# Kernel optimization log

Hardware: AMD Instinct MI355X
Metric: run time of the kernel (lower is better)

Reference implementation:

```python
import jax, jax.numpy as jnp
import numpy as np

D_MODEL = 1024
N_HEADS = 16


def setup_inputs() -> dict:
    key = jax.random.key(0)
    ks = jax.random.split(key, 5)
    B, T, C = 4, 2048, D_MODEL
    x = jax.random.normal(ks[0], (B, T, C), dtype=jnp.float32)
    W_attn = jax.random.normal(ks[1], (C, 3 * C), dtype=jnp.float32) * (1.0 / np.sqrt(C))
    b_attn = jnp.zeros((3 * C,), dtype=jnp.float32)
    W_proj = jax.random.normal(ks[2], (C, C), dtype=jnp.float32) * (1.0 / np.sqrt(C))
    b_proj = jnp.zeros((C,), dtype=jnp.float32)
    return {"x": x, "W_attn": W_attn, "b_attn": b_attn, "W_proj": W_proj, "b_proj": b_proj}


def reference(x, W_attn, b_attn, W_proj, b_proj):
    B, T, C = x.shape
    H = N_HEADS
    hd = C // H
    qkv = x @ W_attn + b_attn                      # [B,T,3C]
    q, k, v = jnp.split(qkv, 3, axis=2)
    # [B,T,C] -> [B,H,T,hd]
    q = q.reshape(B, T, H, hd).transpose(0, 2, 1, 3)
    k = k.reshape(B, T, H, hd).transpose(0, 2, 1, 3)
    v = v.reshape(B, T, H, hd).transpose(0, 2, 1, 3)
    scale = 1.0 / jnp.sqrt(jnp.float32(hd))
    attn = jnp.einsum('bhqd,bhkd->bhqk', q, k) * scale
    causal = jnp.tril(jnp.ones((T, T), dtype=bool))
    attn = jnp.where(causal[None, None], attn, -jnp.inf)
    w = jax.nn.softmax(attn, axis=-1)
    ctx = jnp.einsum('bhqk,bhkd->bhqd', w, v)      # [B,H,T,hd]
    ctx = ctx.transpose(0, 2, 1, 3).reshape(B, T, C)
    return ctx @ W_proj + b_proj
```

## Files before the change

kernel.cpp:

```cpp
#include <hip/hip_runtime.h>
#include <hip/hip_bf16.h>

typedef __bf16 bf16x8 __attribute__((ext_vector_type(8)));
typedef __bf16 bf16x4 __attribute__((ext_vector_type(4)));
typedef float f32x4 __attribute__((ext_vector_type(4)));

#define MFMA(A, B, C) __builtin_amdgcn_mfma_f32_16x16x32_bf16((A), (B), (C), 0, 0, 0)

#if __has_builtin(__builtin_amdgcn_exp2f)
#define EXP2(x) __builtin_amdgcn_exp2f(x)
#else
#define EXP2(x) exp2f(x)
#endif

#define T_SEQ 2048
#define BATCH 4
#define CDIM  1024
#define HEADS 16
#define HD    64
#define MROWS (BATCH * T_SEQ)
#define QK_SCALE 0.18033688011112042f
#define KTILES (CDIM / 64)

__device__ __forceinline__ void async_ld16(const __bf16* g, __bf16* l) {
    __builtin_amdgcn_global_load_lds(
        (const __attribute__((address_space(1))) void*)g,
        (__attribute__((address_space(3))) void*)l, 16, 0, 0);
}

__global__ __launch_bounds__(256) void prep(const float* __restrict__ x,
                                            __bf16* __restrict__ xbf,
                                            const float* __restrict__ Wa,
                                            __bf16* __restrict__ Wat,
                                            const float* __restrict__ Wp,
                                            __bf16* __restrict__ qkv)
{
    __shared__ float tile[32][33];
    const int bid = blockIdx.x;
    if (bid < 4096) {
        long i = ((long)bid * 256 + threadIdx.x) * 8;
        f32x4 f0 = ((const f32x4*)(x + i))[0];
        f32x4 f1 = ((const f32x4*)(x + i))[1];
        bf16x8 v;
#pragma unroll
        for (int j = 0; j < 4; j++) { v[j] = (__bf16)f0[j]; v[4 + j] = (__bf16)f1[j]; }
        *(bf16x8*)(xbf + i) = v;
    } else if (bid < 7168) {
        const int bb = bid - 4096;
        const int tx = threadIdx.x & 31, ty = threadIdx.x >> 5;
        const int c0 = (bb % 96) * 32, r0 = (bb / 96) * 32;
#pragma unroll
        for (int i = 0; i < 4; i++)
            tile[ty + i * 8][tx] = Wa[(long)(r0 + ty + i * 8) * (3 * CDIM) + c0 + tx];
        __syncthreads();
#pragma unroll
        for (int i = 0; i < 4; i++)
            Wat[(long)(c0 + ty + i * 8) * CDIM + r0 + tx] = (__bf16)tile[tx][ty + i * 8];
    } else {
        const int bb = bid - 7168;
        const int tx = threadIdx.x & 31, ty = threadIdx.x >> 5;
        const int c0 = (bb % 32) * 32, r0 = (bb / 32) * 32;
#pragma unroll
        for (int i = 0; i < 4; i++)
            tile[ty + i * 8][tx] = Wp[(long)(r0 + ty + i * 8) * CDIM + c0 + tx];
        __syncthreads();
#pragma unroll
        for (int i = 0; i < 4; i++)
            qkv[(long)(c0 + ty + i * 8) * (3 * CDIM) + 2 * CDIM + r0 + tx] =
                (__bf16)tile[tx][ty + i * 8];
    }
}


#define QS_ALO(p, kt)                                                            \
    do {                                                                         \
        async_ld16(Asrc + (long)(kt) * 64, &Ab[p][sdst]);                        \
        async_ld16(Asrc + (long)128 * CDIM + (kt) * 64, &Ab[p][8192 + sdst]);    \
    } while (0)
#define QS_AHI(p, kt)                                                            \
    do {                                                                         \
        async_ld16(Asrc + (long)64 * CDIM + (kt) * 64, &Ab[p][4096 + sdst]);     \
        async_ld16(Asrc + (long)192 * CDIM + (kt) * 64, &Ab[p][12288 + sdst]);   \
    } while (0)
#define QS_B(p, kt)                                                              \
    do {                                                                         \
        async_ld16(Bsrc + (long)(kt) * 64, &Bb[p][sdst]);                        \
        async_ld16(Bsrc + (long)64 * CDIM + (kt) * 64, &Bb[p][4096 + sdst]);     \
        async_ld16(Bsrc + (long)128 * CDIM + (kt) * 64, &Bb[p][8192 + sdst]);    \
    } while (0)

__global__ __launch_bounds__(512, 2) void gemm_qkv(const __bf16* __restrict__ A,
                                                   const __bf16* __restrict__ Bt,
                                                   const float* __restrict__ bias,
                                                   __bf16* __restrict__ C,
                                                   __bf16* __restrict__ vt)
{
    __shared__ __attribute__((aligned(16))) __bf16 Ab[2][256 * 64];
    __shared__ __attribute__((aligned(16))) __bf16 Bb[2][192 * 64];

    const int bid = (int)blockIdx.x;
    const int swz = (bid & 7) * 64 + (bid >> 3);
    const int n0 = (swz & 15) * 192;
    const int m0 = (swz >> 4) * 256;

    const int t = threadIdx.x;
    const int wave = t >> 6, lane = t & 63;
    const int quad = lane >> 4, l15 = lane & 15;
    const int wm = wave >> 2, wn = wave & 3;

    const int srow = t >> 3;
    const int scol = ((t & 7) * 8) ^ ((srow & 7) << 3);
    const int sdst = srow * 64 + (t & 7) * 8;
    const __bf16* Asrc = A + (long)(m0 + srow) * CDIM + scol;
    const __bf16* Bsrc = Bt + (long)(n0 + srow) * CDIM + scol;

    const int kx0 = (quad * 8) ^ ((l15 & 7) << 3);
    const int kx1 = (32 + quad * 8) ^ ((l15 & 7) << 3);
    const int aro = (wm * 128 + l15) * 64;
    const int bro = (wn * 48 + l15) * 64;

    f32x4 acc[8][3] = {};
    bf16x8 A0[4][2], A1[4][2], B0[2][2], B1[2];

    QS_ALO(0, 0); QS_AHI(0, 0); QS_B(0, 0);
    QS_ALO(1, 1); QS_AHI(1, 1); QS_B(1, 1);
    asm volatile("s_waitcnt vmcnt(7)" ::: "memory");
    __builtin_amdgcn_s_barrier();
#pragma unroll
    for (int mf = 0; mf < 4; mf++) {
        A0[mf][0] = *(const bf16x8*)&Ab[0][aro + mf * 1024 + kx0];
        A0[mf][1] = *(const bf16x8*)&Ab[0][aro + mf * 1024 + kx1];
    }
#pragma unroll
    for (int nf = 0; nf < 2; nf++) {
        B0[nf][0] = *(const bf16x8*)&Bb[0][bro + nf * 1024 + kx0];
        B0[nf][1] = *(const bf16x8*)&Bb[0][bro + nf * 1024 + kx1];
    }

#pragma unroll 2
    for (int kt = 0; kt < KTILES; ++kt) {
        const int cur = kt & 1, nxt = cur ^ 1;

#pragma unroll
        for (int mf = 0; mf < 4; mf++) {
            A1[mf][0] = *(const bf16x8*)&Ab[cur][aro + 4096 + mf * 1024 + kx0];
            A1[mf][1] = *(const bf16x8*)&Ab[cur][aro + 4096 + mf * 1024 + kx1];
        }
        B1[0] = *(const bf16x8*)&Bb[cur][bro + 2048 + kx0];
        B1[1] = *(const bf16x8*)&Bb[cur][bro + 2048 + kx1];
        asm volatile("s_waitcnt lgkmcnt(10)" ::: "memory");
        __builtin_amdgcn_sched_barrier(0);
        __builtin_amdgcn_s_setprio(1);
#pragma unroll
        for (int mf = 0; mf < 4; mf++)
#pragma unroll
            for (int nf = 0; nf < 2; nf++) {
                acc[mf][nf] = MFMA(A0[mf][0], B0[nf][0], acc[mf][nf]);
                acc[mf][nf] = MFMA(A0[mf][1], B0[nf][1], acc[mf][nf]);
            }
        __builtin_amdgcn_s_setprio(0);
        asm volatile("s_waitcnt lgkmcnt(0)" ::: "memory");
        __builtin_amdgcn_sched_barrier(0);
        __builtin_amdgcn_s_setprio(1);
#pragma unroll
        for (int mf = 0; mf < 4; mf++)
#pragma unroll
            for (int nf = 0; nf < 2; nf++) {
                acc[4 + mf][nf] = MFMA(A1[mf][0], B0[nf][0], acc[4 + mf][nf]);
                acc[4 + mf][nf] = MFMA(A1[mf][1], B0[nf][1], acc[4 + mf][nf]);
            }
        __builtin_amdgcn_s_setprio(0);
        asm volatile("s_waitcnt vmcnt(0)" ::: "memory");
        __builtin_amdgcn_s_barrier();

        __builtin_amdgcn_s_setprio(1);
#pragma unroll
        for (int mf = 0; mf < 4; mf++) {
            acc[mf][2] = MFMA(A0[mf][0], B1[0], acc[mf][2]);
            acc[mf][2] = MFMA(A0[mf][1], B1[1], acc[mf][2]);
        }
        __builtin_amdgcn_s_setprio(0);
        if (kt + 1 < KTILES) {
#pragma unroll
            for (int mf = 0; mf < 4; mf++) {
                A0[mf][0] = *(const bf16x8*)&Ab[nxt][aro + mf * 1024 + kx0];
                A0[mf][1] = *(const bf16x8*)&Ab[nxt][aro + mf * 1024 + kx1];
            }
#pragma unroll
            for (int nf = 0; nf < 2; nf++) {
                B0[nf][0] = *(const bf16x8*)&Bb[nxt][bro + nf * 1024 + kx0];
                B0[nf][1] = *(const bf16x8*)&Bb[nxt][bro + nf * 1024 + kx1];
            }
        }
        if (kt + 2 < KTILES) { QS_ALO(cur, kt + 2); QS_AHI(cur, kt + 2); QS_B(cur, kt + 2); }
        __builtin_amdgcn_s_setprio(1);
#pragma unroll
        for (int mf = 0; mf < 4; mf++) {
            acc[4 + mf][2] = MFMA(A1[mf][0], B1[0], acc[4 + mf][2]);
            acc[4 + mf][2] = MFMA(A1[mf][1], B1[1], acc[4 + mf][2]);
        }
        __builtin_amdgcn_s_setprio(0);
    }

    const int bB = m0 >> 11;
    const int tb = (m0 & (T_SEQ - 1)) + wm * 128;
#pragma unroll
    for (int mf = 0; mf < 8; mf++) {
#pragma unroll
        for (int nf = 0; nf < 3; nf++) {
            const int colb = n0 + wn * 48 + nf * 16;
            const int col = colb + l15;
            const float bv = bias[col];
            if (colb >= 2 * CDIM) {
                __bf16* vdst = vt + (long)(bB * CDIM + col - 2 * CDIM) * T_SEQ
                             + tb + (mf >> 2) * 64 + (mf & 3) * 16 + quad * 4;
                bf16x4 pv;
#pragma unroll
                for (int r = 0; r < 4; r++) pv[r] = (__bf16)(acc[mf][nf][r] + bv);
                *(bf16x4*)vdst = pv;
            } else {
                const float sc = (col < CDIM) ? QK_SCALE : 1.0f;
#pragma unroll
                for (int r = 0; r < 4; r++) {
                    const int row = m0 + wm * 128 + (mf >> 2) * 64 + (mf & 3) * 16 + quad * 4 + r;
                    C[(long)row * (3 * CDIM) + col] = (__bf16)((acc[mf][nf][r] + bv) * sc);
                }
            }
        }
    }
}

#define PS_A(p, kt)                                                              \
    do {                                                                         \
        async_ld16(Asrc + (long)(kt) * 64, &Ab[p][sdst]);                        \
        async_ld16(Asrc + (long)64 * (3 * CDIM) + (kt) * 64, &Ab[p][4096 + sdst]); \
    } while (0)
#define PS_B(p, kt)                                                              \
    do {                                                                         \
        async_ld16(Bsrc + (long)(kt) * 64, &Bb[p][sdst]);                        \
        async_ld16(Bsrc + (long)64 * (3 * CDIM) + (kt) * 64, &Bb[p][4096 + sdst]); \
        async_ld16(Bsrc + (long)128 * (3 * CDIM) + (kt) * 64, &Bb[p][8192 + sdst]); \
        async_ld16(Bsrc + (long)192 * (3 * CDIM) + (kt) * 64, &Bb[p][12288 + sdst]); \
    } while (0)

__global__ __launch_bounds__(512, 2) void gemm_proj(const __bf16* __restrict__ A,
                                                    const float* __restrict__ bias,
                                                    float* __restrict__ C)
{
    __shared__ __attribute__((aligned(16))) __bf16 Ab[2][128 * 64];
    __shared__ __attribute__((aligned(16))) __bf16 Bb[2][256 * 64];

    const int bid = (int)blockIdx.x;
    const int swz = (bid & 7) * 32 + (bid >> 3);
    const int n0 = (swz & 3) * 256;
    const int m0 = (swz >> 2) * 128;

    const int t = threadIdx.x;
    const int wave = t >> 6, lane = t & 63;
    const int quad = lane >> 4, l15 = lane & 15;
    const int wm = wave >> 2, wn = wave & 3;

    const int srow = t >> 3;
    const int scol = ((t & 7) * 8) ^ ((srow & 7) << 3);
    const int sdst = srow * 64 + (t & 7) * 8;
    const __bf16* Asrc = A + (long)(m0 + srow) * (3 * CDIM) + scol;
    const __bf16* Bsrc = A + (long)(n0 + srow) * (3 * CDIM) + 2 * CDIM + scol;

    const int kx0 = (quad * 8) ^ ((l15 & 7) << 3);
    const int kx1 = (32 + quad * 8) ^ ((l15 & 7) << 3);
    const int aro = (wm * 64 + l15) * 64;
    const int bro = (wn * 64 + l15) * 64;

    f32x4 acc[4][4] = {};
    bf16x8 A0[2][2], A1[2][2], B0[2][2], B1[2][2];

    PS_A(0, 0); PS_B(0, 0);
    PS_A(1, 1); PS_B(1, 1);
    asm volatile("s_waitcnt vmcnt(6)" ::: "memory");
    __builtin_amdgcn_s_barrier();
#pragma unroll
    for (int mf = 0; mf < 2; mf++) {
        A0[mf][0] = *(const bf16x8*)&Ab[0][aro + mf * 1024 + kx0];
        A0[mf][1] = *(const bf16x8*)&Ab[0][aro + mf * 1024 + kx1];
    }
#pragma unroll
    for (int nf = 0; nf < 2; nf++) {
        B0[nf][0] = *(const bf16x8*)&Bb[0][bro + nf * 1024 + kx0];
        B0[nf][1] = *(const bf16x8*)&Bb[0][bro + nf * 1024 + kx1];
    }

#pragma unroll 2
    for (int kt = 0; kt < KTILES; ++kt) {
        const int cur = kt & 1, nxt = cur ^ 1;

#pragma unroll
        for (int mf = 0; mf < 2; mf++) {
            A1[mf][0] = *(const bf16x8*)&Ab[cur][aro + 2048 + mf * 1024 + kx0];
            A1[mf][1] = *(const bf16x8*)&Ab[cur][aro + 2048 + mf * 1024 + kx1];
        }
#pragma unroll
        for (int nf = 0; nf < 2; nf++) {
            B1[nf][0] = *(const bf16x8*)&Bb[cur][bro + 2048 + nf * 1024 + kx0];
            B1[nf][1] = *(const bf16x8*)&Bb[cur][bro + 2048 + nf * 1024 + kx1];
        }
        asm volatile("s_waitcnt lgkmcnt(8)" ::: "memory");
        __builtin_amdgcn_sched_barrier(0);
        __builtin_amdgcn_s_setprio(1);
#pragma unroll
        for (int mf = 0; mf < 2; mf++)
#pragma unroll
            for (int nf = 0; nf < 2; nf++) {
                acc[mf][nf] = MFMA(A0[mf][0], B0[nf][0], acc[mf][nf]);
                acc[mf][nf] = MFMA(A0[mf][1], B0[nf][1], acc[mf][nf]);
            }
        __builtin_amdgcn_s_setprio(0);
        asm volatile("s_waitcnt lgkmcnt(0)" ::: "memory");
        __builtin_amdgcn_sched_barrier(0);
        __builtin_amdgcn_s_setprio(1);
#pragma unroll
        for (int mf = 0; mf < 2; mf++)
#pragma unroll
            for (int nf = 0; nf < 2; nf++) {
                acc[2 + mf][nf] = MFMA(A1[mf][0], B0[nf][0], acc[2 + mf][nf]);
                acc[2 + mf][nf] = MFMA(A1[mf][1], B0[nf][1], acc[2 + mf][nf]);
            }
        __builtin_amdgcn_s_setprio(0);
        asm volatile("s_waitcnt vmcnt(0)" ::: "memory");
        __builtin_amdgcn_s_barrier();

        __builtin_amdgcn_s_setprio(1);
#pragma unroll
        for (int mf = 0; mf < 2; mf++)
#pragma unroll
            for (int nf = 0; nf < 2; nf++) {
                acc[mf][2 + nf] = MFMA(A0[mf][0], B1[nf][0], acc[mf][2 + nf]);
                acc[mf][2 + nf] = MFMA(A0[mf][1], B1[nf][1], acc[mf][2 + nf]);
            }
        __builtin_amdgcn_s_setprio(0);
        if (kt + 1 < KTILES) {
#pragma unroll
            for (int mf = 0; mf < 2; mf++) {
                A0[mf][0] = *(const bf16x8*)&Ab[nxt][aro + mf * 1024 + kx0];
                A0[mf][1] = *(const bf16x8*)&Ab[nxt][aro + mf * 1024 + kx1];
            }
#pragma unroll
            for (int nf = 0; nf < 2; nf++) {
                B0[nf][0] = *(const bf16x8*)&Bb[nxt][bro + nf * 1024 + kx0];
                B0[nf][1] = *(const bf16x8*)&Bb[nxt][bro + nf * 1024 + kx1];
            }
        }
        if (kt + 2 < KTILES) { PS_A(cur, kt + 2); PS_B(cur, kt + 2); }
        __builtin_amdgcn_s_setprio(1);
#pragma unroll
        for (int mf = 0; mf < 2; mf++)
#pragma unroll
            for (int nf = 0; nf < 2; nf++) {
                acc[2 + mf][2 + nf] = MFMA(A1[mf][0], B1[nf][0], acc[2 + mf][2 + nf]);
                acc[2 + mf][2 + nf] = MFMA(A1[mf][1], B1[nf][1], acc[2 + mf][2 + nf]);
            }
        __builtin_amdgcn_s_setprio(0);
    }

#pragma unroll
    for (int mf = 0; mf < 4; mf++) {
#pragma unroll
        for (int nf = 0; nf < 4; nf++) {
            const int col = n0 + wn * 64 + (nf >> 1) * 32 + (nf & 1) * 16 + l15;
            const float bv = bias[col];
#pragma unroll
            for (int r = 0; r < 4; r++) {
                const int row = m0 + wm * 64 + (mf >> 1) * 32 + (mf & 1) * 16 + quad * 4 + r;
                C[(long)row * CDIM + col] = acc[mf][nf][r] + bv;
            }
        }
    }
}

#define ATT_STAGE(p, kt_)                                                        \
    do {                                                                         \
        const __bf16* kp_ = kbase + (long)(kt_) * 64 * (3 * CDIM);               \
        async_ld16(kp_,      &Ks[p][0][t * 8]);                                  \
        async_ld16(kp_ + 32, &Ks[p][1][t * 8]);                                  \
        const __bf16* vp_ = vbase + (kt_) * 64;                                  \
        async_ld16(vp_,      &Vts[p][0][t * 8]);                                 \
        async_ld16(vp_ + 32, &Vts[p][1][t * 8]);                                 \
    } while (0)

__global__ __launch_bounds__(256, 3) void attn_kernel(__bf16* qkv,
                                                      const __bf16* __restrict__ vt)
{
    __shared__ __attribute__((aligned(16))) __bf16 Ks[2][2][64 * 32];
    __shared__ __attribute__((aligned(16))) __bf16 Vts[2][2][64 * 32];
    __shared__ __attribute__((aligned(16))) __bf16 Ps[8][16 * 72];

    const int bh = blockIdx.x;
    const int b = bh >> 4, h = bh & 15;
    const int qt = (int)gridDim.y - 1 - (int)blockIdx.y;
    const int q0 = qt * 128;
    const int t = threadIdx.x;
    const int wave = t >> 6, lane = t & 63;
    const int quad = lane >> 4, l15 = lane & 15;

    bf16x8 qfr[2][2];
#pragma unroll
    for (int f = 0; f < 2; f++) {
        const __bf16* qb = qkv + (long)(b * T_SEQ + q0 + f * 64 + wave * 16 + l15) * (3 * CDIM) + h * HD;
        qfr[f][0] = *(const bf16x8*)(qb + quad * 8);
        qfr[f][1] = *(const bf16x8*)(qb + 32 + quad * 8);
    }

    bf16x8 vone;
#pragma unroll
    for (int j = 0; j < 8; j++) vone[j] = (__bf16)1.0f;

    f32x4 Oacc[2][4] = {};
    f32x4 lacc[2] = {};

    const __bf16* kbase = qkv + (long)(b * T_SEQ + (t >> 2)) * (3 * CDIM)
                          + CDIM + h * HD + (t & 3) * 8;
    const __bf16* vbase = vt + ((long)bh * HD + (t >> 2)) * T_SEQ + (t & 3) * 8;

    const int ntiles = (q0 + 128) / 64;

    ATT_STAGE(0, 0);
    ATT_STAGE(1, 1);
    asm volatile("s_waitcnt vmcnt(4)" ::: "memory");
    __builtin_amdgcn_s_barrier();

    for (int kt = 0; kt < ntiles; kt++) {
        const int cur = kt & 1;

#pragma unroll
        for (int c = 0; c < 4; c++) {
            bf16x8 kf0 = *(const bf16x8*)&Ks[cur][0][(c * 16 + l15) * 32 + quad * 8];
            bf16x8 kf1 = *(const bf16x8*)&Ks[cur][1][(c * 16 + l15) * 32 + quad * 8];
#pragma unroll
            for (int f = 0; f < 2; f++) {
                f32x4 z = {};
                z = MFMA(kf0, qfr[f][0], z);
                z = MFMA(kf1, qfr[f][1], z);
                const int qbf = q0 + f * 64 + wave * 16;
                const int qg = qbf + l15;
                const int kvb = kt * 64 + c * 16 + quad * 4;
                bf16x4 pk;
                if (kt * 64 + 63 > qbf) {
#pragma unroll
                    for (int r = 0; r < 4; r++) {
                        float v = (kvb + r > qg) ? -1e30f : z[r];
                        pk[r] = (__bf16)EXP2(v);
                    }
                } else {
#pragma unroll
                    for (int r = 0; r < 4; r++)
                        pk[r] = (__bf16)EXP2(z[r]);
                }
                *(bf16x4*)&Ps[wave * 2 + f][l15 * 72 + c * 16 + quad * 4] = pk;
            }
        }

        __threadfence_block();

        bf16x8 pf[2][2];
#pragma unroll
        for (int f = 0; f < 2; f++) {
            pf[f][0] = *(const bf16x8*)&Ps[wave * 2 + f][l15 * 72 + quad * 8];
            pf[f][1] = *(const bf16x8*)&Ps[wave * 2 + f][l15 * 72 + 32 + quad * 8];
        }
        bf16x8 vf[4][2];
#pragma unroll
        for (int n = 0; n < 4; n++) {
            vf[n][0] = *(const bf16x8*)&Vts[cur][0][(n * 16 + l15) * 32 + quad * 8];
            vf[n][1] = *(const bf16x8*)&Vts[cur][1][(n * 16 + l15) * 32 + quad * 8];
        }
        asm volatile("s_waitcnt lgkmcnt(0)" ::: "memory");
        __builtin_amdgcn_sched_barrier(0);
        asm volatile("s_waitcnt vmcnt(0)" ::: "memory");
        __builtin_amdgcn_s_barrier();

        if (kt + 2 < ntiles) ATT_STAGE(cur, kt + 2);
        __builtin_amdgcn_s_setprio(1);
#pragma unroll
        for (int f = 0; f < 2; f++) {
            lacc[f] = MFMA(pf[f][0], vone, lacc[f]);
            lacc[f] = MFMA(pf[f][1], vone, lacc[f]);
        }
#pragma unroll
        for (int n = 0; n < 4; n++)
#pragma unroll
            for (int f = 0; f < 2; f++) {
                Oacc[f][n] = MFMA(pf[f][0], vf[n][0], Oacc[f][n]);
                Oacc[f][n] = MFMA(pf[f][1], vf[n][1], Oacc[f][n]);
            }
        __builtin_amdgcn_s_setprio(0);
    }

#pragma unroll
    for (int f = 0; f < 2; f++)
#pragma unroll
        for (int n = 0; n < 4; n++) {
            int col = h * HD + n * 16 + l15;
#pragma unroll
            for (int r = 0; r < 4; r++) {
                int row = q0 + f * 64 + wave * 16 + quad * 4 + r;
                float val = Oacc[f][n][r] / lacc[f][r];
                qkv[(long)(b * T_SEQ + row) * (3 * CDIM) + col] = (__bf16)val;
            }
        }
}

extern "C" void kernel_launch(void* const* d_in, const int* in_sizes, int n_in,
                              void* d_out, int out_size, void* d_ws, size_t ws_size,
                              hipStream_t stream) {
    (void)in_sizes; (void)n_in; (void)out_size; (void)ws_size;
    const float* x  = (const float*)d_in[0];
    const float* Wa = (const float*)d_in[1];
    const float* ba = (const float*)d_in[2];
    const float* Wp = (const float*)d_in[3];
    const float* bp = (const float*)d_in[4];
    float* out = (float*)d_out;

    char* ws = (char*)d_ws;
    __bf16* qkv = (__bf16*)(ws);
    __bf16* vt  = (__bf16*)(ws + 50331648);
    __bf16* xbf = (__bf16*)d_out;
    __bf16* Wat = (__bf16*)((char*)d_out + 16777216);

    prep<<<dim3(8192), 256, 0, stream>>>(x, xbf, Wa, Wat, Wp, qkv);

    gemm_qkv<<<dim3(512), 512, 0, stream>>>(xbf, Wat, ba, qkv, vt);

    attn_kernel<<<dim3(BATCH * HEADS, T_SEQ / 128), 256, 0, stream>>>(qkv, vt);

    gemm_proj<<<dim3(256), 512, 0, stream>>>(qkv, bp, out);
}
```

Measured before the change: 229.4 us.

## Restructure GEMM LDS fragment prefetch to load full next tile after MFMAs

In both the QKV and projection GEMM main loops, the per-iteration LDS fragment reads are rescheduled. The high half (A1/B1) of the next k-tile is now read together with the low half at the end of the previous iteration instead of at the top of the current one. The last two MFMA groups are merged into one block after the barrier, and the lgkmcnt waits are relaxed so only part of the fragments must arrive before the second MFMA group. The aim is to overlap LDS read latency with MFMA work. The cost is higher register pressure and LDS reads sitting directly after the barrier without MFMAs to interleave.

```diff
diff --git a/kernel.cpp b/kernel.cpp
--- a/kernel.cpp
+++ b/kernel.cpp
@@ -89,6 +89,30 @@
         async_ld16(Bsrc + (long)128 * CDIM + (kt) * 64, &Bb[p][8192 + sdst]);    \
     } while (0)
 
+#define Q_READ_LO(buf)                                                           \
+    do {                                                                         \
+        _Pragma("unroll")                                                        \
+        for (int mf = 0; mf < 4; mf++) {                                         \
+            A0[mf][0] = *(const bf16x8*)&Ab[buf][aro + mf * 1024 + kx0];         \
+            A0[mf][1] = *(const bf16x8*)&Ab[buf][aro + mf * 1024 + kx1];         \
+        }                                                                        \
+        _Pragma("unroll")                                                        \
+        for (int nf = 0; nf < 2; nf++) {                                         \
+            B0[nf][0] = *(const bf16x8*)&Bb[buf][bro + nf * 1024 + kx0];         \
+            B0[nf][1] = *(const bf16x8*)&Bb[buf][bro + nf * 1024 + kx1];         \
+        }                                                                        \
+    } while (0)
+#define Q_READ_HI(buf)                                                           \
+    do {                                                                         \
+        _Pragma("unroll")                                                        \
+        for (int mf = 0; mf < 4; mf++) {                                         \
+            A1[mf][0] = *(const bf16x8*)&Ab[buf][aro + 4096 + mf * 1024 + kx0];  \
+            A1[mf][1] = *(const bf16x8*)&Ab[buf][aro + 4096 + mf * 1024 + kx1];  \
+        }                                                                        \
+        B1[0] = *(const bf16x8*)&Bb[buf][bro + 2048 + kx0];                      \
+        B1[1] = *(const bf16x8*)&Bb[buf][bro + 2048 + kx1];                      \
+    } while (0)
+
 __global__ __launch_bounds__(512, 2) void gemm_qkv(const __bf16* __restrict__ A,
                                                    const __bf16* __restrict__ Bt,
                                                    const float* __restrict__ bias,
@@ -126,28 +150,13 @@
     QS_ALO(1, 1); QS_AHI(1, 1); QS_B(1, 1);
     asm volatile("s_waitcnt vmcnt(7)" ::: "memory");
     __builtin_amdgcn_s_barrier();
-#pragma unroll
-    for (int mf = 0; mf < 4; mf++) {
-        A0[mf][0] = *(const bf16x8*)&Ab[0][aro + mf * 1024 + kx0];
-        A0[mf][1] = *(const bf16x8*)&Ab[0][aro + mf * 1024 + kx1];
-    }
-#pragma unroll
-    for (int nf = 0; nf < 2; nf++) {
-        B0[nf][0] = *(const bf16x8*)&Bb[0][bro + nf * 1024 + kx0];
-        B0[nf][1] = *(const bf16x8*)&Bb[0][bro + nf * 1024 + kx1];
-    }
+    Q_READ_LO(0);
+    Q_READ_HI(0);
 
 #pragma unroll 2
     for (int kt = 0; kt < KTILES; ++kt) {
         const int cur = kt & 1, nxt = cur ^ 1;
 
-#pragma unroll
-        for (int mf = 0; mf < 4; mf++) {
-            A1[mf][0] = *(const bf16x8*)&Ab[cur][aro + 4096 + mf * 1024 + kx0];
-            A1[mf][1] = *(const bf16x8*)&Ab[cur][aro + 4096 + mf * 1024 + kx1];
-        }
-        B1[0] = *(const bf16x8*)&Bb[cur][bro + 2048 + kx0];
-        B1[1] = *(const bf16x8*)&Bb[cur][bro + 2048 + kx1];
         asm volatile("s_waitcnt lgkmcnt(10)" ::: "memory");
         __builtin_amdgcn_sched_barrier(0);
         __builtin_amdgcn_s_setprio(1);
@@ -159,7 +168,7 @@
                 acc[mf][nf] = MFMA(A0[mf][1], B0[nf][1], acc[mf][nf]);
             }
         __builtin_amdgcn_s_setprio(0);
-        asm volatile("s_waitcnt lgkmcnt(0)" ::: "memory");
+        asm volatile("s_waitcnt lgkmcnt(2)" ::: "memory");
         __builtin_amdgcn_sched_barrier(0);
         __builtin_amdgcn_s_setprio(1);
 #pragma unroll
@@ -173,33 +182,22 @@
         asm volatile("s_waitcnt vmcnt(0)" ::: "memory");
         __builtin_amdgcn_s_barrier();
 
+        asm volatile("s_waitcnt lgkmcnt(0)" ::: "memory");
+        __builtin_amdgcn_sched_barrier(0);
         __builtin_amdgcn_s_setprio(1);
 #pragma unroll
         for (int mf = 0; mf < 4; mf++) {
             acc[mf][2] = MFMA(A0[mf][0], B1[0], acc[mf][2]);
             acc[mf][2] = MFMA(A0[mf][1], B1[1], acc[mf][2]);
-        }
-        __builtin_amdgcn_s_setprio(0);
-        if (kt + 1 < KTILES) {
-#pragma unroll
-            for (int mf = 0; mf < 4; mf++) {
-                A0[mf][0] = *(const bf16x8*)&Ab[nxt][aro + mf * 1024 + kx0];
-                A0[mf][1] = *(const bf16x8*)&Ab[nxt][aro + mf * 1024 + kx1];
-            }
-#pragma unroll
-            for (int nf = 0; nf < 2; nf++) {
-                B0[nf][0] = *(const bf16x8*)&Bb[nxt][bro + nf * 1024 + kx0];
-                B0[nf][1] = *(const bf16x8*)&Bb[nxt][bro + nf * 1024 + kx1];
-            }
-        }
-        if (kt + 2 < KTILES) { QS_ALO(cur, kt + 2); QS_AHI(cur, kt + 2); QS_B(cur, kt + 2); }
-        __builtin_amdgcn_s_setprio(1);
-#pragma unroll
-        for (int mf = 0; mf < 4; mf++) {
             acc[4 + mf][2] = MFMA(A1[mf][0], B1[0], acc[4 + mf][2]);
             acc[4 + mf][2] = MFMA(A1[mf][1], B1[1], acc[4 + mf][2]);
         }
         __builtin_amdgcn_s_setprio(0);
+        if (kt + 1 < KTILES) {
+            Q_READ_LO(nxt);
+            Q_READ_HI(nxt);
+        }
+        if (kt + 2 < KTILES) { QS_ALO(cur, kt + 2); QS_AHI(cur, kt + 2); QS_B(cur, kt + 2); }
     }
 
     const int bB = m0 >> 11;
@@ -243,6 +241,33 @@
         async_ld16(Bsrc + (long)192 * (3 * CDIM) + (kt) * 64, &Bb[p][12288 + sdst]); \
     } while (0)
 
+#define P_READ_LO(buf)                                                           \
+    do {                                                                         \
+        _Pragma("unroll")                                                        \
+        for (int mf = 0; mf < 2; mf++) {                                         \
+            A0[mf][0] = *(const bf16x8*)&Ab[buf][aro + mf * 1024 + kx0];         \
+            A0[mf][1] = *(const bf16x8*)&Ab[buf][aro + mf * 1024 + kx1];         \
+        }                                                                        \
+        _Pragma("unroll")                                                        \
+        for (int nf = 0; nf < 2; nf++) {                                         \
+            B0[nf][0] = *(const bf16x8*)&Bb[buf][bro + nf * 1024 + kx0];         \
+            B0[nf][1] = *(const bf16x8*)&Bb[buf][bro + nf * 1024 + kx1];         \
+        }                                                                        \
+    } while (0)
+#define P_READ_HI(buf)                                                           \
+    do {                                                                         \
+        _Pragma("unroll")                                                        \
+        for (int mf = 0; mf < 2; mf++) {                                         \
+            A1[mf][0] = *(const bf16x8*)&Ab[buf][aro + 2048 + mf * 1024 + kx0];  \
+            A1[mf][1] = *(const bf16x8*)&Ab[buf][aro + 2048 + mf * 1024 + kx1];  \
+        }                                                                        \
+        _Pragma("unroll")                                                        \
+        for (int nf = 0; nf < 2; nf++) {                                         \
+            B1[nf][0] = *(const bf16x8*)&Bb[buf][bro + 2048 + nf * 1024 + kx0];  \
+            B1[nf][1] = *(const bf16x8*)&Bb[buf][bro + 2048 + nf * 1024 + kx1];  \
+        }                                                                        \
+    } while (0)
+
 __global__ __launch_bounds__(512, 2) void gemm_proj(const __bf16* __restrict__ A,
                                                     const float* __restrict__ bias,
                                                     float* __restrict__ C)
@@ -278,31 +303,13 @@
     PS_A(1, 1); PS_B(1, 1);
     asm volatile("s_waitcnt vmcnt(6)" ::: "memory");
     __builtin_amdgcn_s_barrier();
-#pragma unroll
-    for (int mf = 0; mf < 2; mf++) {
-        A0[mf][0] = *(const bf16x8*)&Ab[0][aro + mf * 1024 + kx0];
-        A0[mf][1] = *(const bf16x8*)&Ab[0][aro + mf * 1024 + kx1];
-    }
-#pragma unroll
-    for (int nf = 0; nf < 2; nf++) {
-        B0[nf][0] = *(const bf16x8*)&Bb[0][bro + nf * 1024 + kx0];
-        B0[nf][1] = *(const bf16x8*)&Bb[0][bro + nf * 1024 + kx1];
-    }
+    P_READ_LO(0);
+    P_READ_HI(0);
 
 #pragma unroll 2
     for (int kt = 0; kt < KTILES; ++kt) {
         const int cur = kt & 1, nxt = cur ^ 1;
 
-#pragma unroll
-        for (int mf = 0; mf < 2; mf++) {
-            A1[mf][0] = *(const bf16x8*)&Ab[cur][aro + 2048 + mf * 1024 + kx0];
-            A1[mf][1] = *(const bf16x8*)&Ab[cur][aro + 2048 + mf * 1024 + kx1];
-        }
-#pragma unroll
-        for (int nf = 0; nf < 2; nf++) {
-            B1[nf][0] = *(const bf16x8*)&Bb[cur][bro + 2048 + nf * 1024 + kx0];
-            B1[nf][1] = *(const bf16x8*)&Bb[cur][bro + 2048 + nf * 1024 + kx1];
-        }
         asm volatile("s_waitcnt lgkmcnt(8)" ::: "memory");
         __builtin_amdgcn_sched_barrier(0);
         __builtin_amdgcn_s_setprio(1);
@@ -314,7 +321,7 @@
                 acc[mf][nf] = MFMA(A0[mf][1], B0[nf][1], acc[mf][nf]);
             }
         __builtin_amdgcn_s_setprio(0);
-        asm volatile("s_waitcnt lgkmcnt(0)" ::: "memory");
+        asm volatile("s_waitcnt lgkmcnt(4)" ::: "memory");
         __builtin_amdgcn_sched_barrier(0);
         __builtin_amdgcn_s_setprio(1);
 #pragma unroll
@@ -328,6 +335,8 @@
         asm volatile("s_waitcnt vmcnt(0)" ::: "memory");
         __builtin_amdgcn_s_barrier();
 
+        asm volatile("s_waitcnt lgkmcnt(0)" ::: "memory");
+        __builtin_amdgcn_sched_barrier(0);
         __builtin_amdgcn_s_setprio(1);
 #pragma unroll
         for (int mf = 0; mf < 2; mf++)
@@ -335,30 +344,15 @@
             for (int nf = 0; nf < 2; nf++) {
                 acc[mf][2 + nf] = MFMA(A0[mf][0], B1[nf][0], acc[mf][2 + nf]);
                 acc[mf][2 + nf] = MFMA(A0[mf][1], B1[nf][1], acc[mf][2 + nf]);
-            }
-        __builtin_amdgcn_s_setprio(0);
-        if (kt + 1 < KTILES) {
-#pragma unroll
-            for (int mf = 0; mf < 2; mf++) {
-                A0[mf][0] = *(const bf16x8*)&Ab[nxt][aro + mf * 1024 + kx0];
-                A0[mf][1] = *(const bf16x8*)&Ab[nxt][aro + mf * 1024 + kx1];
-            }
-#pragma unroll
-            for (int nf = 0; nf < 2; nf++) {
-                B0[nf][0] = *(const bf16x8*)&Bb[nxt][bro + nf * 1024 + kx0];
-                B0[nf][1] = *(const bf16x8*)&Bb[nxt][bro + nf * 1024 + kx1];
-            }
-        }
-        if (kt + 2 < KTILES) { PS_A(cur, kt + 2); PS_B(cur, kt + 2); }
-        __builtin_amdgcn_s_setprio(1);
-#pragma unroll
-        for (int mf = 0; mf < 2; mf++)
-#pragma unroll
-            for (int nf = 0; nf < 2; nf++) {
                 acc[2 + mf][2 + nf] = MFMA(A1[mf][0], B1[nf][0], acc[2 + mf][2 + nf]);
                 acc[2 + mf][2 + nf] = MFMA(A1[mf][1], B1[nf][1], acc[2 + mf][2 + nf]);
             }
         __builtin_amdgcn_s_setprio(0);
+        if (kt + 1 < KTILES) {
+            P_READ_LO(nxt);
+            P_READ_HI(nxt);
+        }
+        if (kt + 2 < KTILES) { PS_A(cur, kt + 2); PS_B(cur, kt + 2); }
     }
 
 #pragma unroll
```

After: 234.3 us. 2.2% more time.
